# Performance work log

Measured on AMD Instinct MI355X. Metric: run time of the kernel, lower is better.

The kernel has to match this reference:

```python
import jax, jax.numpy as jnp
import numpy as np
import math

B, L, D = 2, 2048, 1024
H, KV, HD = 16, 4, 64          # num_heads, num_kv_heads, head_dim
GROUPS = H // KV
ROPE_BASE = 10000.0


def _alibi_slopes(n_heads):
    def pow2(n):
        start = 2.0 ** (-(2.0 ** (-(math.log2(n) - 3))))
        return [start * (start ** i) for i in range(n)]
    if math.log2(n_heads).is_integer():
        return pow2(n_heads)
    c = 2 ** math.floor(math.log2(n_heads))
    return pow2(c) + _alibi_slopes(2 * c)[0::2][: n_heads - c]


def _rope_cos_sin(seq_len, dim, dtype):
    inv_freq = 1.0 / (ROPE_BASE ** (jnp.arange(0, dim, 2, dtype=jnp.float32) / dim))
    t = jnp.arange(seq_len, dtype=jnp.float32)
    freqs = t[:, None] * inv_freq[None, :]          # [L, dim/2]
    emb = jnp.concatenate([freqs, freqs], axis=-1)  # [L, dim]
    return jnp.cos(emb).astype(dtype), jnp.sin(emb).astype(dtype)


def _rotate_half(x):
    x1, x2 = x[..., : x.shape[-1] // 2], x[..., x.shape[-1] // 2 :]
    return jnp.concatenate([-x2, x1], axis=-1)


def setup_inputs() -> dict:
    key = jax.random.key(0)
    ks = jax.random.split(key, 5)
    s = 0.02
    return {
        "x": jax.random.normal(ks[0], (B, L, D), jnp.float32),
        "Wq": jax.random.normal(ks[1], (D, H * HD), jnp.float32) * s,
        "Wk": jax.random.normal(ks[2], (D, KV * HD), jnp.float32) * s,
        "Wv": jax.random.normal(ks[3], (D, KV * HD), jnp.float32) * s,
        "Wo": jax.random.normal(ks[4], (H * HD, D), jnp.float32) * s,
    }


def reference(x, Wq, Wk, Wv, Wo):
    b, l, _ = x.shape
    q = (x @ Wq).reshape(b, l, H, HD).transpose(0, 2, 1, 3)   # [B,H,L,hd]
    k = (x @ Wk).reshape(b, l, KV, HD).transpose(0, 2, 1, 3)  # [B,KV,L,hd]
    v = (x @ Wv).reshape(b, l, KV, HD).transpose(0, 2, 1, 3)
    # MQA broadcast: repeat_interleave over head dim
    k = jnp.repeat(k, GROUPS, axis=1)  # [B,H,L,hd]
    v = jnp.repeat(v, GROUPS, axis=1)

    cos, sin = _rope_cos_sin(l, HD, x.dtype)  # [L,hd]
    q = q * cos + _rotate_half(q) * sin
    k = k * cos + _rotate_half(k) * sin

    attn = jnp.einsum("bhqd,bhkd->bhqk", q, k) / math.sqrt(HD)
    # ALiBi bias: (j - i) * slope_h
    pos = jnp.arange(l)
    rel = (pos[None, :] - pos[:, None]).astype(x.dtype)        # [L,L]
    slopes = jnp.asarray(_alibi_slopes(H), dtype=x.dtype)      # [H]
    attn = attn + slopes[None, :, None, None] * rel[None, None, :, :]

    attn = jax.nn.softmax(attn, axis=-1)
    out = jnp.einsum("bhqk,bhkd->bhqd", attn, v)               # [B,H,L,hd]
    out = out.transpose(0, 2, 1, 3).reshape(b, l, H * HD)
    return out @ Wo
```

## Files before the change

kernel.cpp:

```cpp
#include <hip/hip_runtime.h>
#include <math.h>

typedef unsigned short u16;
typedef unsigned int u32;
typedef __attribute__((ext_vector_type(8))) short short8;
typedef __attribute__((ext_vector_type(4))) short short4v;
typedef __attribute__((ext_vector_type(4))) float floatx4;
typedef __attribute__((ext_vector_type(2))) unsigned int uint2v;

#define HN 16
#define KVN 4
#define HDN 64
#define BN_ 2
#define LN 2048
#define DN 1024

__device__ __forceinline__ u16 f2bf(float f) {
    u32 u = __float_as_uint(f);
    u32 r = (u + 0x7fffu + ((u >> 16) & 1u)) >> 16;
    return (u16)r;
}

__device__ __forceinline__ u32 pack2bf(float f0, float f1) {
    u32 u0 = __float_as_uint(f0);
    u32 u1 = __float_as_uint(f1);
    u0 += 0x7fffu + ((u0 >> 16) & 1u);
    u1 += 0x7fffu + ((u1 >> 16) & 1u);
    return __builtin_amdgcn_perm(u1, u0, 0x07060302u);
}

__device__ __forceinline__ void gl16(const u16* g, u16* l) {
    __builtin_amdgcn_global_load_lds(
        (const __attribute__((address_space(1))) u32*)g,
        (__attribute__((address_space(3))) u32*)l, 16, 0, 0);
}

__device__ __forceinline__ void do_transpose(const float* __restrict__ W, u16* __restrict__ WT,
                                             int R, int C, int bx, int by, int tid,
                                             float (*t)[33]) {
    int tx = tid & 31, ty = tid >> 5;
    int c0 = bx * 32, r0 = by * 32;
#pragma unroll
    for (int i = 0; i < 4; i++) {
        int r = r0 + ty + i * 8;
        t[ty + i * 8][tx] = W[(size_t)r * C + c0 + tx];
    }
    __syncthreads();
#pragma unroll
    for (int i = 0; i < 4; i++) {
        int c = c0 + ty + i * 8;
        WT[(size_t)c * R + r0 + tx] = f2bf(t[tx][ty + i * 8]);
    }
}

__global__ __launch_bounds__(256) void prep_kernel(const float* __restrict__ x,
                                                   const float* __restrict__ Wq,
                                                   const float* __restrict__ Wk,
                                                   const float* __restrict__ Wv,
                                                   const float* __restrict__ Wo,
                                                   u16* __restrict__ xb,
                                                   u16* __restrict__ WT,
                                                   u16* __restrict__ WoT) {
    __shared__ float t[32][33];
    int blk = blockIdx.x, tid = threadIdx.x;
    if (blk < 4096) {
        int i = blk * 256 + tid;
        floatx4 v = ((const floatx4*)x)[i];
        short4v o;
        o[0] = (short)f2bf(v[0]);
        o[1] = (short)f2bf(v[1]);
        o[2] = (short)f2bf(v[2]);
        o[3] = (short)f2bf(v[3]);
        ((short4v*)xb)[i] = o;
    } else if (blk < 5120) {
        int z = blk - 4096;
        do_transpose(Wq, WT, 1024, 1024, z & 31, z >> 5, tid, t);
    } else if (blk < 5376) {
        int z = blk - 5120;
        do_transpose(Wk, WT + 1024 * 1024, 1024, 256, z & 7, z >> 3, tid, t);
    } else if (blk < 5632) {
        int z = blk - 5376;
        do_transpose(Wv, WT + 1280 * 1024, 1024, 256, z & 7, z >> 3, tid, t);
    } else {
        int z = blk - 5632;
        do_transpose(Wo, WoT, 1024, 1024, z & 31, z >> 5, tid, t);
    }
}

__global__ __launch_bounds__(256) void gemm_qkv_rope(const u16* __restrict__ A,
                                                     const u16* __restrict__ BT,
                                                     u16* __restrict__ Qb,
                                                     u16* __restrict__ Kb,
                                                     u16* __restrict__ Vt) {
    __shared__ u16 sm[16384];
    const int K = 1024;
    int tid = threadIdx.x;
    int w = tid >> 6, l = tid & 63, quad = l >> 4, l16 = l & 15;
    int wm = (w >> 1) * 64, wn = (w & 1) * 64;
    floatx4 acc[4][4];
#pragma unroll
    for (int i = 0; i < 4; i++)
#pragma unroll
        for (int j = 0; j < 4; j++) acc[i][j] = (floatx4){0.f, 0.f, 0.f, 0.f};
    const u16* ag0 = A + (size_t)(blockIdx.y * 128 + (tid >> 2)) * K + (tid & 3) * 8;
    const u16* ag1 = ag0 + (size_t)64 * K;
    const u16* bg0 = BT + (size_t)(blockIdx.x * 128 + (tid >> 2)) * K + (tid & 3) * 8;
    const u16* bg1 = bg0 + (size_t)64 * K;
    int lbase = tid * 8;
    gl16(ag0, &sm[lbase]);
    gl16(ag1, &sm[2048 + lbase]);
    gl16(bg0, &sm[4096 + lbase]);
    gl16(bg1, &sm[6144 + lbase]);
    for (int it = 0; it < 32; it++) {
        __syncthreads();
        int cur = it & 1;
        if (it + 1 < 32) {
            int nb = (cur ^ 1) * 8192;
            ag0 += 32; ag1 += 32; bg0 += 32; bg1 += 32;
            gl16(ag0, &sm[nb + lbase]);
            gl16(ag1, &sm[nb + 2048 + lbase]);
            gl16(bg0, &sm[nb + 4096 + lbase]);
            gl16(bg1, &sm[nb + 6144 + lbase]);
        }
        const u16* sa = &sm[cur * 8192];
        const u16* sb = sa + 4096;
        short8 af[4], bfr[4];
#pragma unroll
        for (int mt = 0; mt < 4; mt++) af[mt] = *(const short8*)&sa[(wm + mt * 16 + l16) * 32 + quad * 8];
#pragma unroll
        for (int nt = 0; nt < 4; nt++) bfr[nt] = *(const short8*)&sb[(wn + nt * 16 + l16) * 32 + quad * 8];
#pragma unroll
        for (int mt = 0; mt < 4; mt++)
#pragma unroll
            for (int nt = 0; nt < 4; nt++)
                acc[mt][nt] = __builtin_amdgcn_mfma_f32_16x16x32_bf16(af[mt], bfr[nt], acc[mt][nt], 0, 0, 0);
    }
    int bx = blockIdx.x;
    int row0 = blockIdx.y * 128 + wm;
    const float L2R32 = 0.4152410118609203f;
    if (bx < 10) {
        int isK = (bx >= 8);
        int head = isK ? ((bx - 8) * 2 + (w & 1)) : (bx * 2 + (w & 1));
        u16* dst = isK ? (Kb + ((size_t)head) * LN * HDN) : (Qb + ((size_t)head) * LN * HDN);
        size_t bstride = (size_t)(isK ? KVN : HN) * LN * HDN;
        float invf[2];
#pragma unroll
        for (int ntp = 0; ntp < 2; ntp++) invf[ntp] = exp2f(-(float)(ntp * 16 + l16) * L2R32);
#pragma unroll
        for (int mt = 0; mt < 4; mt++)
#pragma unroll
            for (int r = 0; r < 4; r++) {
                int row = row0 + mt * 16 + quad * 4 + r;
                int b = row >> 11;
                int lpos = row & 2047;
                float lf = (float)lpos;
#pragma unroll
                for (int ntp = 0; ntp < 2; ntp++) {
                    float th = lf * invf[ntp];
                    float s, c;
                    __sincosf(th, &s, &c);
                    float x1 = acc[mt][ntp][r], x2 = acc[mt][ntp + 2][r];
                    size_t base = (size_t)b * bstride + ((size_t)lpos) * HDN + ntp * 16 + l16;
                    dst[base] = f2bf(x1 * c - x2 * s);
                    dst[base + 32] = f2bf(x2 * c + x1 * s);
                }
            }
    } else {
        int kv = (bx - 10) * 2 + (w & 1);
#pragma unroll
        for (int mt = 0; mt < 4; mt++)
#pragma unroll
            for (int r = 0; r < 4; r++) {
                int row = row0 + mt * 16 + quad * 4 + r;
                int b = row >> 11;
                int lpos = row & 2047;
#pragma unroll
                for (int nt = 0; nt < 4; nt++) {
                    int d = nt * 16 + l16;
                    Vt[(((size_t)b * KVN + kv) * HDN + d) * LN + lpos] = f2bf(acc[mt][nt][r]);
                }
            }
    }
}

__global__ __launch_bounds__(256) void gemm_bf16_f32(const u16* __restrict__ A,
                                                     const u16* __restrict__ BT,
                                                     float* __restrict__ C,
                                                     int M, int N, int K) {
    __shared__ u16 sm[12288];
    int tid = threadIdx.x;
    int w = tid >> 6, l = tid & 63, quad = l >> 4, l16 = l & 15;
    int wm = (w >> 1) * 64, wn = (w & 1) * 32;
    floatx4 acc[4][2];
#pragma unroll
    for (int i = 0; i < 4; i++)
#pragma unroll
        for (int j = 0; j < 2; j++) acc[i][j] = (floatx4){0.f, 0.f, 0.f, 0.f};
    const u16* ag0 = A + (size_t)(blockIdx.y * 128 + 16 * w + (l >> 2)) * K + (l & 3) * 8;
    const u16* ag1 = ag0 + (size_t)64 * K;
    const u16* bg = BT + (size_t)(blockIdx.x * 64 + 16 * w + (l >> 2)) * K + (l & 3) * 8;
    int lbase = w * 512 + l * 8;
    gl16(ag0, &sm[lbase]);
    gl16(ag1, &sm[2048 + lbase]);
    gl16(bg, &sm[4096 + lbase]);
    int nit = K >> 5;
    for (int it = 0; it < nit; it++) {
        __syncthreads();
        int cur = it & 1;
        if (it + 1 < nit) {
            int nb = (cur ^ 1) * 6144;
            ag0 += 32; ag1 += 32; bg += 32;
            gl16(ag0, &sm[nb + lbase]);
            gl16(ag1, &sm[nb + 2048 + lbase]);
            gl16(bg, &sm[nb + 4096 + lbase]);
        }
        const u16* smc = &sm[cur * 6144];
        short8 af[4], bfr[2];
#pragma unroll
        for (int mt = 0; mt < 4; mt++) af[mt] = *(const short8*)&smc[(wm + mt * 16 + l16) * 32 + quad * 8];
#pragma unroll
        for (int nt = 0; nt < 2; nt++) bfr[nt] = *(const short8*)&smc[4096 + (wn + nt * 16 + l16) * 32 + quad * 8];
#pragma unroll
        for (int mt = 0; mt < 4; mt++)
#pragma unroll
            for (int nt = 0; nt < 2; nt++)
                acc[mt][nt] = __builtin_amdgcn_mfma_f32_16x16x32_bf16(af[mt], bfr[nt], acc[mt][nt], 0, 0, 0);
    }
#pragma unroll
    for (int mt = 0; mt < 4; mt++)
#pragma unroll
        for (int nt = 0; nt < 2; nt++)
#pragma unroll
            for (int r = 0; r < 4; r++) {
                int row = blockIdx.y * 128 + wm + mt * 16 + quad * 4 + r;
                int col = blockIdx.x * 64 + wn + nt * 16 + l16;
                C[(size_t)row * N + col] = acc[mt][nt][r];
            }
}

static __device__ const signed char hs_tab[16] = {15, 14, 13, 12, 11, 10, 9, 8,
                                                  0, 1, 2, 3, 4, 5, 6, 7};
static __device__ const signed char nit_tab[16] = {32, 32, 32, 32, 32, 24, 17, 12,
                                                   1, 2, 2, 3, 3, 5, 6, 9};

__global__ __launch_bounds__(256) void attention_kernel(const u16* __restrict__ Qb,
                                                        const u16* __restrict__ Kb,
                                                        const u16* __restrict__ Vt,
                                                        u16* __restrict__ AO) {
    __shared__ u16 sm[20992];
    int rank = blockIdx.x >> 5, sub = blockIdx.x & 31;
    int h = hs_tab[rank], nit = nit_tab[rank];
    int ks0 = LN - nit * 64;
    int b = sub >> 4, qb = sub & 15;
    int kv = h >> 2;
    int tid = threadIdx.x, w = tid >> 6, l = tid & 63, quad = l >> 4, l16 = l & 15;
    const u16* Kbase = Kb + (((size_t)b * KVN + kv) * LN) * HDN;
    const u16* Vbase = Vt + (((size_t)b * KVN + kv) * HDN) * LN;
    short8 bq[2][2];
#pragma unroll
    for (int t = 0; t < 2; t++) {
        const u16* Qrow = Qb + (((size_t)b * HN + h) * LN + qb * 128 + t * 64 + w * 16 + l16) * HDN;
        bq[t][0] = *(const short8*)&Qrow[quad * 8];
        bq[t][1] = *(const short8*)&Qrow[32 + quad * 8];
    }
    const float LOG2E = 1.4426950408889634f;
    float sLE = exp2f(-0.5f * (float)(h + 1)) * LOG2E;
    float c1 = 0.125f * LOG2E;
    float koff[4][4];
#pragma unroll
    for (int nt = 0; nt < 4; nt++)
#pragma unroll
        for (int r = 0; r < 4; r++)
            koff[nt][r] = fmaf(sLE, (float)(ks0 + nt * 16 + quad * 4 + r - (LN - 1)), -17.312340491f);
    float kbrun = 0.0f, kstep = 64.0f * sLE;
    floatx4 O[2][4], lacc[2];
#pragma unroll
    for (int t = 0; t < 2; t++) {
        lacc[t] = (floatx4){0.f, 0.f, 0.f, 0.f};
#pragma unroll
        for (int md = 0; md < 4; md++) O[t][md] = (floatx4){0.f, 0.f, 0.f, 0.f};
    }
    short8 ones;
#pragma unroll
    for (int z = 0; z < 8; z++) ones[z] = (short)0x3F80;
    u16* pb = &sm[16384 + w * 1152];
    int lbase = w * 512 + l * 8;
    const u16* kg = Kbase + (size_t)(ks0 + 16 * w + (l >> 2)) * 64 + (l & 3) * 8;
    const u16* vg = Vbase + (size_t)(16 * w + (l >> 2)) * 2048 + ks0 + (l & 3) * 8;
    gl16(kg, &sm[lbase]);
    gl16(kg + 32, &sm[2048 + lbase]);
    gl16(vg, &sm[8192 + lbase]);
    gl16(vg + 32, &sm[8192 + 2048 + lbase]);
    for (int it = 0; it < nit; it++) {
        __syncthreads();
        int cur = it & 1;
        if (it + 1 < nit) {
            int nb = (cur ^ 1) * 4096;
            kg += 4096;
            vg += 64;
            gl16(kg, &sm[nb + lbase]);
            gl16(kg + 32, &sm[nb + 2048 + lbase]);
            gl16(vg, &sm[8192 + nb + lbase]);
            gl16(vg + 32, &sm[8192 + nb + 2048 + lbase]);
        }
        const u16* kc = &sm[cur * 4096];
        const u16* vc = &sm[8192 + cur * 4096];
        short8 ak0[4], ak1[4], av0[4], av1[4];
#pragma unroll
        for (int nt = 0; nt < 4; nt++) {
            ak0[nt] = *(const short8*)&kc[(nt * 16 + l16) * 32 + quad * 8];
            ak1[nt] = *(const short8*)&kc[2048 + (nt * 16 + l16) * 32 + quad * 8];
        }
#pragma unroll
        for (int md = 0; md < 4; md++) {
            av0[md] = *(const short8*)&vc[(md * 16 + l16) * 32 + quad * 8];
            av1[md] = *(const short8*)&vc[2048 + (md * 16 + l16) * 32 + quad * 8];
        }
        float koff2[4][4];
#pragma unroll
        for (int nt = 0; nt < 4; nt++)
#pragma unroll
            for (int r = 0; r < 4; r++) koff2[nt][r] = koff[nt][r] + kbrun;
        kbrun += kstep;
#pragma unroll
        for (int t = 0; t < 2; t++) {
            floatx4 S[4];
#pragma unroll
            for (int nt = 0; nt < 4; nt++) {
                floatx4 sa = (floatx4){0.f, 0.f, 0.f, 0.f};
                sa = __builtin_amdgcn_mfma_f32_16x16x32_bf16(ak0[nt], bq[t][0], sa, 0, 0, 0);
                sa = __builtin_amdgcn_mfma_f32_16x16x32_bf16(ak1[nt], bq[t][1], sa, 0, 0, 0);
                S[nt] = sa;
            }
#pragma unroll
            for (int nt = 0; nt < 4; nt++) {
                float p0 = __builtin_amdgcn_exp2f(S[nt][0] * c1 + koff2[nt][0]);
                float p1 = __builtin_amdgcn_exp2f(S[nt][1] * c1 + koff2[nt][1]);
                float p2 = __builtin_amdgcn_exp2f(S[nt][2] * c1 + koff2[nt][2]);
                float p3 = __builtin_amdgcn_exp2f(S[nt][3] * c1 + koff2[nt][3]);
                uint2v pk;
                pk[0] = pack2bf(p0, p1);
                pk[1] = pack2bf(p2, p3);
                *(uint2v*)&pb[l16 * 72 + nt * 16 + quad * 4] = pk;
            }
            short8 bp0 = *(const short8*)&pb[l16 * 72 + quad * 8];
            short8 bp1 = *(const short8*)&pb[l16 * 72 + 32 + quad * 8];
#pragma unroll
            for (int md = 0; md < 4; md++) {
                O[t][md] = __builtin_amdgcn_mfma_f32_16x16x32_bf16(av0[md], bp0, O[t][md], 0, 0, 0);
                O[t][md] = __builtin_amdgcn_mfma_f32_16x16x32_bf16(av1[md], bp1, O[t][md], 0, 0, 0);
            }
            lacc[t] = __builtin_amdgcn_mfma_f32_16x16x32_bf16(ones, bp0, lacc[t], 0, 0, 0);
            lacc[t] = __builtin_amdgcn_mfma_f32_16x16x32_bf16(ones, bp1, lacc[t], 0, 0, 0);
        }
    }
#pragma unroll
    for (int t = 0; t < 2; t++) {
        float inv = 1.0f / lacc[t][0];
        int qg = qb * 128 + t * 64 + w * 16 + l16;
        size_t base = ((size_t)b * LN + qg) * 1024 + h * 64 + quad * 4;
#pragma unroll
        for (int md = 0; md < 4; md++) {
            uint2v pk;
            pk[0] = pack2bf(O[t][md][0] * inv, O[t][md][1] * inv);
            pk[1] = pack2bf(O[t][md][2] * inv, O[t][md][3] * inv);
            *(uint2v*)&AO[base + md * 16] = pk;
        }
    }
}

extern "C" void kernel_launch(void* const* d_in, const int* in_sizes, int n_in,
                              void* d_out, int out_size, void* d_ws, size_t ws_size,
                              hipStream_t stream) {
    const float* x = (const float*)d_in[0];
    const float* Wq = (const float*)d_in[1];
    const float* Wk = (const float*)d_in[2];
    const float* Wv = (const float*)d_in[3];
    const float* Wo = (const float*)d_in[4];
    float* out = (float*)d_out;
    char* ws = (char*)d_ws;
    u16* xb = (u16*)(ws);
    u16* WT = (u16*)(ws + 8388608);
    u16* WoT = (u16*)(ws + 11534336);
    u16* Qb = (u16*)(ws + 13631488);
    u16* Kb = (u16*)(ws + 22020096);
    u16* Vt = (u16*)(ws + 24117248);
    u16* AO = xb;

    prep_kernel<<<6656, 256, 0, stream>>>(x, Wq, Wk, Wv, Wo, xb, WT, WoT);
    gemm_qkv_rope<<<dim3(12, 32), 256, 0, stream>>>(xb, WT, Qb, Kb, Vt);
    attention_kernel<<<512, 256, 0, stream>>>(Qb, Kb, Vt, AO);
    gemm_bf16_f32<<<dim3(1024 / 64, 4096 / 128), 256, 0, stream>>>(AO, WoT, out, 4096, 1024, 1024);
}
```

Baseline: 163.1 us.

## Halve tile sizes in QKV GEMM and attention to double block counts

The QKV+RoPE GEMM moves from 128x128 to 128x64 tiles, so each block owns one head and the grid has 768 blocks instead of 384. The attention kernel now handles 64 query rows per block instead of 128, launching 1024 blocks. The output GEMM switches from a 2x2 to a 4x1 wave layout. The aim is better CU occupancy and load balance on a large GPU, at the cost of reloading K/V and weight tiles more often per output.

```diff
diff --git a/kernel.cpp b/kernel.cpp
--- a/kernel.cpp
+++ b/kernel.cpp
@@ -92,45 +92,42 @@
                                                      u16* __restrict__ Qb,
                                                      u16* __restrict__ Kb,
                                                      u16* __restrict__ Vt) {
-    __shared__ u16 sm[16384];
+    __shared__ u16 sm[12288];
     const int K = 1024;
     int tid = threadIdx.x;
     int w = tid >> 6, l = tid & 63, quad = l >> 4, l16 = l & 15;
-    int wm = (w >> 1) * 64, wn = (w & 1) * 64;
-    floatx4 acc[4][4];
-#pragma unroll
-    for (int i = 0; i < 4; i++)
+    int wm = w * 32;
+    floatx4 acc[2][4];
+#pragma unroll
+    for (int i = 0; i < 2; i++)
 #pragma unroll
         for (int j = 0; j < 4; j++) acc[i][j] = (floatx4){0.f, 0.f, 0.f, 0.f};
     const u16* ag0 = A + (size_t)(blockIdx.y * 128 + (tid >> 2)) * K + (tid & 3) * 8;
     const u16* ag1 = ag0 + (size_t)64 * K;
-    const u16* bg0 = BT + (size_t)(blockIdx.x * 128 + (tid >> 2)) * K + (tid & 3) * 8;
-    const u16* bg1 = bg0 + (size_t)64 * K;
+    const u16* bg = BT + (size_t)(blockIdx.x * 64 + (tid >> 2)) * K + (tid & 3) * 8;
     int lbase = tid * 8;
     gl16(ag0, &sm[lbase]);
     gl16(ag1, &sm[2048 + lbase]);
-    gl16(bg0, &sm[4096 + lbase]);
-    gl16(bg1, &sm[6144 + lbase]);
+    gl16(bg, &sm[4096 + lbase]);
     for (int it = 0; it < 32; it++) {
         __syncthreads();
         int cur = it & 1;
         if (it + 1 < 32) {
-            int nb = (cur ^ 1) * 8192;
-            ag0 += 32; ag1 += 32; bg0 += 32; bg1 += 32;
+            int nb = (cur ^ 1) * 6144;
+            ag0 += 32; ag1 += 32; bg += 32;
             gl16(ag0, &sm[nb + lbase]);
             gl16(ag1, &sm[nb + 2048 + lbase]);
-            gl16(bg0, &sm[nb + 4096 + lbase]);
-            gl16(bg1, &sm[nb + 6144 + lbase]);
-        }
-        const u16* sa = &sm[cur * 8192];
+            gl16(bg, &sm[nb + 4096 + lbase]);
+        }
+        const u16* sa = &sm[cur * 6144];
         const u16* sb = sa + 4096;
-        short8 af[4], bfr[4];
-#pragma unroll
-        for (int mt = 0; mt < 4; mt++) af[mt] = *(const short8*)&sa[(wm + mt * 16 + l16) * 32 + quad * 8];
-#pragma unroll
-        for (int nt = 0; nt < 4; nt++) bfr[nt] = *(const short8*)&sb[(wn + nt * 16 + l16) * 32 + quad * 8];
-#pragma unroll
-        for (int mt = 0; mt < 4; mt++)
+        short8 af[2], bfr[4];
+#pragma unroll
+        for (int mt = 0; mt < 2; mt++) af[mt] = *(const short8*)&sa[(wm + mt * 16 + l16) * 32 + quad * 8];
+#pragma unroll
+        for (int nt = 0; nt < 4; nt++) bfr[nt] = *(const short8*)&sb[(nt * 16 + l16) * 32 + quad * 8];
+#pragma unroll
+        for (int mt = 0; mt < 2; mt++)
 #pragma unroll
             for (int nt = 0; nt < 4; nt++)
                 acc[mt][nt] = __builtin_amdgcn_mfma_f32_16x16x32_bf16(af[mt], bfr[nt], acc[mt][nt], 0, 0, 0);
@@ -138,16 +135,17 @@
     int bx = blockIdx.x;
     int row0 = blockIdx.y * 128 + wm;
     const float L2R32 = 0.4152410118609203f;
-    if (bx < 10) {
-        int isK = (bx >= 8);
-        int head = isK ? ((bx - 8) * 2 + (w & 1)) : (bx * 2 + (w & 1));
-        u16* dst = isK ? (Kb + ((size_t)head) * LN * HDN) : (Qb + ((size_t)head) * LN * HDN);
+    if (bx < 20) {
+        int isK = (bx >= 16);
+        int head = isK ? (bx - 16) : bx;
+        u16* dst = isK ? Kb : Qb;
         size_t bstride = (size_t)(isK ? KVN : HN) * LN * HDN;
         float invf[2];
 #pragma unroll
         for (int ntp = 0; ntp < 2; ntp++) invf[ntp] = exp2f(-(float)(ntp * 16 + l16) * L2R32);
-#pragma unroll
-        for (int mt = 0; mt < 4; mt++)
+        dst += (size_t)head * LN * HDN;
+#pragma unroll
+        for (int mt = 0; mt < 2; mt++)
 #pragma unroll
             for (int r = 0; r < 4; r++) {
                 int row = row0 + mt * 16 + quad * 4 + r;
@@ -166,9 +164,9 @@
                 }
             }
     } else {
-        int kv = (bx - 10) * 2 + (w & 1);
-#pragma unroll
-        for (int mt = 0; mt < 4; mt++)
+        int kv = bx - 20;
+#pragma unroll
+        for (int mt = 0; mt < 2; mt++)
 #pragma unroll
             for (int r = 0; r < 4; r++) {
                 int row = row0 + mt * 16 + quad * 4 + r;
@@ -183,59 +181,60 @@
     }
 }
 
-__global__ __launch_bounds__(256) void gemm_bf16_f32(const u16* __restrict__ A,
-                                                     const u16* __restrict__ BT,
-                                                     float* __restrict__ C,
-                                                     int M, int N, int K) {
+__global__ __launch_bounds__(256) void gemm_out(const u16* __restrict__ A,
+                                                const u16* __restrict__ BT,
+                                                float* __restrict__ C) {
     __shared__ u16 sm[12288];
+    const int K = 1024, N = 1024;
     int tid = threadIdx.x;
     int w = tid >> 6, l = tid & 63, quad = l >> 4, l16 = l & 15;
-    int wm = (w >> 1) * 64, wn = (w & 1) * 32;
-    floatx4 acc[4][2];
-#pragma unroll
-    for (int i = 0; i < 4; i++)
-#pragma unroll
-        for (int j = 0; j < 2; j++) acc[i][j] = (floatx4){0.f, 0.f, 0.f, 0.f};
-    const u16* ag0 = A + (size_t)(blockIdx.y * 128 + 16 * w + (l >> 2)) * K + (l & 3) * 8;
+    int wm = w * 32;
+    floatx4 acc[2][4];
+#pragma unroll
+    for (int i = 0; i < 2; i++)
+#pragma unroll
+        for (int j = 0; j < 4; j++) acc[i][j] = (floatx4){0.f, 0.f, 0.f, 0.f};
+    const u16* ag0 = A + (size_t)(blockIdx.y * 128 + (tid >> 2)) * K + (tid & 3) * 8;
     const u16* ag1 = ag0 + (size_t)64 * K;
-    const u16* bg = BT + (size_t)(blockIdx.x * 64 + 16 * w + (l >> 2)) * K + (l & 3) * 8;
-    int lbase = w * 512 + l * 8;
+    const u16* bg = BT + (size_t)(blockIdx.x * 64 + (tid >> 2)) * K + (tid & 3) * 8;
+    int lbase = tid * 8;
     gl16(ag0, &sm[lbase]);
     gl16(ag1, &sm[2048 + lbase]);
     gl16(bg, &sm[4096 + lbase]);
-    int nit = K >> 5;
-    for (int it = 0; it < nit; it++) {
+    for (int it = 0; it < 32; it++) {
         __syncthreads();
         int cur = it & 1;
-        if (it + 1 < nit) {
+        if (it + 1 < 32) {
             int nb = (cur ^ 1) * 6144;
             ag0 += 32; ag1 += 32; bg += 32;
             gl16(ag0, &sm[nb + lbase]);
             gl16(ag1, &sm[nb + 2048 + lbase]);
             gl16(bg, &sm[nb + 4096 + lbase]);
         }
-        const u16* smc = &sm[cur * 6144];
-        short8 af[4], bfr[2];
-#pragma unroll
-        for (int mt = 0; mt < 4; mt++) af[mt] = *(const short8*)&smc[(wm + mt * 16 + l16) * 32 + quad * 8];
-#pragma unroll
-        for (int nt = 0; nt < 2; nt++) bfr[nt] = *(const short8*)&smc[4096 + (wn + nt * 16 + l16) * 32 + quad * 8];
-#pragma unroll
-        for (int mt = 0; mt < 4; mt++)
-#pragma unroll
-            for (int nt = 0; nt < 2; nt++)
+        const u16* sa = &sm[cur * 6144];
+        const u16* sb = sa + 4096;
+        short8 af[2], bfr[4];
+#pragma unroll
+        for (int mt = 0; mt < 2; mt++) af[mt] = *(const short8*)&sa[(wm + mt * 16 + l16) * 32 + quad * 8];
+#pragma unroll
+        for (int nt = 0; nt < 4; nt++) bfr[nt] = *(const short8*)&sb[(nt * 16 + l16) * 32 + quad * 8];
+#pragma unroll
+        for (int mt = 0; mt < 2; mt++)
+#pragma unroll
+            for (int nt = 0; nt < 4; nt++)
                 acc[mt][nt] = __builtin_amdgcn_mfma_f32_16x16x32_bf16(af[mt], bfr[nt], acc[mt][nt], 0, 0, 0);
     }
 #pragma unroll
-    for (int mt = 0; mt < 4; mt++)
-#pragma unroll
-        for (int nt = 0; nt < 2; nt++)
-#pragma unroll
-            for (int r = 0; r < 4; r++) {
-                int row = blockIdx.y * 128 + wm + mt * 16 + quad * 4 + r;
-                int col = blockIdx.x * 64 + wn + nt * 16 + l16;
+    for (int mt = 0; mt < 2; mt++)
+#pragma unroll
+        for (int r = 0; r < 4; r++) {
+            int row = blockIdx.y * 128 + wm + mt * 16 + quad * 4 + r;
+#pragma unroll
+            for (int nt = 0; nt < 4; nt++) {
+                int col = blockIdx.x * 64 + nt * 16 + l16;
                 C[(size_t)row * N + col] = acc[mt][nt][r];
             }
+        }
 }
 
 static __device__ const signed char hs_tab[16] = {15, 14, 13, 12, 11, 10, 9, 8,
@@ -248,21 +247,17 @@
                                                         const u16* __restrict__ Vt,
                                                         u16* __restrict__ AO) {
     __shared__ u16 sm[20992];
-    int rank = blockIdx.x >> 5, sub = blockIdx.x & 31;
+    int rank = blockIdx.x >> 6, sub = blockIdx.x & 63;
     int h = hs_tab[rank], nit = nit_tab[rank];
     int ks0 = LN - nit * 64;
-    int b = sub >> 4, qb = sub & 15;
+    int b = sub >> 5, qb = sub & 31;
     int kv = h >> 2;
     int tid = threadIdx.x, w = tid >> 6, l = tid & 63, quad = l >> 4, l16 = l & 15;
     const u16* Kbase = Kb + (((size_t)b * KVN + kv) * LN) * HDN;
     const u16* Vbase = Vt + (((size_t)b * KVN + kv) * HDN) * LN;
-    short8 bq[2][2];
-#pragma unroll
-    for (int t = 0; t < 2; t++) {
-        const u16* Qrow = Qb + (((size_t)b * HN + h) * LN + qb * 128 + t * 64 + w * 16 + l16) * HDN;
-        bq[t][0] = *(const short8*)&Qrow[quad * 8];
-        bq[t][1] = *(const short8*)&Qrow[32 + quad * 8];
-    }
+    const u16* Qrow = Qb + (((size_t)b * HN + h) * LN + qb * 64 + w * 16 + l16) * HDN;
+    short8 bq0 = *(const short8*)&Qrow[quad * 8];
+    short8 bq1 = *(const short8*)&Qrow[32 + quad * 8];
     const float LOG2E = 1.4426950408889634f;
     float sLE = exp2f(-0.5f * (float)(h + 1)) * LOG2E;
     float c1 = 0.125f * LOG2E;
@@ -273,13 +268,10 @@
         for (int r = 0; r < 4; r++)
             koff[nt][r] = fmaf(sLE, (float)(ks0 + nt * 16 + quad * 4 + r - (LN - 1)), -17.312340491f);
     float kbrun = 0.0f, kstep = 64.0f * sLE;
-    floatx4 O[2][4], lacc[2];
-#pragma unroll
-    for (int t = 0; t < 2; t++) {
-        lacc[t] = (floatx4){0.f, 0.f, 0.f, 0.f};
-#pragma unroll
-        for (int md = 0; md < 4; md++) O[t][md] = (floatx4){0.f, 0.f, 0.f, 0.f};
-    }
+    floatx4 O[4], lacc;
+    lacc = (floatx4){0.f, 0.f, 0.f, 0.f};
+#pragma unroll
+    for (int md = 0; md < 4; md++) O[md] = (floatx4){0.f, 0.f, 0.f, 0.f};
     short8 ones;
 #pragma unroll
     for (int z = 0; z < 8; z++) ones[z] = (short)0x3F80;
@@ -316,56 +308,45 @@
             av0[md] = *(const short8*)&vc[(md * 16 + l16) * 32 + quad * 8];
             av1[md] = *(const short8*)&vc[2048 + (md * 16 + l16) * 32 + quad * 8];
         }
-        float koff2[4][4];
-#pragma unroll
-        for (int nt = 0; nt < 4; nt++)
-#pragma unroll
-            for (int r = 0; r < 4; r++) koff2[nt][r] = koff[nt][r] + kbrun;
+        floatx4 S[4];
+#pragma unroll
+        for (int nt = 0; nt < 4; nt++) {
+            floatx4 sa = (floatx4){0.f, 0.f, 0.f, 0.f};
+            sa = __builtin_amdgcn_mfma_f32_16x16x32_bf16(ak0[nt], bq0, sa, 0, 0, 0);
+            sa = __builtin_amdgcn_mfma_f32_16x16x32_bf16(ak1[nt], bq1, sa, 0, 0, 0);
+            S[nt] = sa;
+        }
+#pragma unroll
+        for (int nt = 0; nt < 4; nt++) {
+            float p0 = __builtin_amdgcn_exp2f(S[nt][0] * c1 + (koff[nt][0] + kbrun));
+            float p1 = __builtin_amdgcn_exp2f(S[nt][1] * c1 + (koff[nt][1] + kbrun));
+            float p2 = __builtin_amdgcn_exp2f(S[nt][2] * c1 + (koff[nt][2] + kbrun));
+            float p3 = __builtin_amdgcn_exp2f(S[nt][3] * c1 + (koff[nt][3] + kbrun));
+            uint2v pk;
+            pk[0] = pack2bf(p0, p1);
+            pk[1] = pack2bf(p2, p3);
+            *(uint2v*)&pb[l16 * 72 + nt * 16 + quad * 4] = pk;
+        }
         kbrun += kstep;
-#pragma unroll
-        for (int t = 0; t < 2; t++) {
-            floatx4 S[4];
-#pragma unroll
-            for (int nt = 0; nt < 4; nt++) {
-                floatx4 sa = (floatx4){0.f, 0.f, 0.f, 0.f};
-                sa = __builtin_amdgcn_mfma_f32_16x16x32_bf16(ak0[nt], bq[t][0], sa, 0, 0, 0);
-                sa = __builtin_amdgcn_mfma_f32_16x16x32_bf16(ak1[nt], bq[t][1], sa, 0, 0, 0);
-                S[nt] = sa;
-            }
-#pragma unroll
-            for (int nt = 0; nt < 4; nt++) {
-                float p0 = __builtin_amdgcn_exp2f(S[nt][0] * c1 + koff2[nt][0]);
-                float p1 = __builtin_amdgcn_exp2f(S[nt][1] * c1 + koff2[nt][1]);
-                float p2 = __builtin_amdgcn_exp2f(S[nt][2] * c1 + koff2[nt][2]);
-                float p3 = __builtin_amdgcn_exp2f(S[nt][3] * c1 + koff2[nt][3]);
-                uint2v pk;
-                pk[0] = pack2bf(p0, p1);
-                pk[1] = pack2bf(p2, p3);
-                *(uint2v*)&pb[l16 * 72 + nt * 16 + quad * 4] = pk;
-            }
-            short8 bp0 = *(const short8*)&pb[l16 * 72 + quad * 8];
-            short8 bp1 = *(const short8*)&pb[l16 * 72 + 32 + quad * 8];
-#pragma unroll
-            for (int md = 0; md < 4; md++) {
-                O[t][md] = __builtin_amdgcn_mfma_f32_16x16x32_bf16(av0[md], bp0, O[t][md], 0, 0, 0);
-                O[t][md] = __builtin_amdgcn_mfma_f32_16x16x32_bf16(av1[md], bp1, O[t][md], 0, 0, 0);
-            }
-            lacc[t] = __builtin_amdgcn_mfma_f32_16x16x32_bf16(ones, bp0, lacc[t], 0, 0, 0);
-            lacc[t] = __builtin_amdgcn_mfma_f32_16x16x32_bf16(ones, bp1, lacc[t], 0, 0, 0);
-        }
-    }
-#pragma unroll
-    for (int t = 0; t < 2; t++) {
-        float inv = 1.0f / lacc[t][0];
-        int qg = qb * 128 + t * 64 + w * 16 + l16;
-        size_t base = ((size_t)b * LN + qg) * 1024 + h * 64 + quad * 4;
+        short8 bp0 = *(const short8*)&pb[l16 * 72 + quad * 8];
+        short8 bp1 = *(const short8*)&pb[l16 * 72 + 32 + quad * 8];
 #pragma unroll
         for (int md = 0; md < 4; md++) {
-            uint2v pk;
-            pk[0] = pack2bf(O[t][md][0] * inv, O[t][md][1] * inv);
-            pk[1] = pack2bf(O[t][md][2] * inv, O[t][md][3] * inv);
-            *(uint2v*)&AO[base + md * 16] = pk;
-        }
+            O[md] = __builtin_amdgcn_mfma_f32_16x16x32_bf16(av0[md], bp0, O[md], 0, 0, 0);
+            O[md] = __builtin_amdgcn_mfma_f32_16x16x32_bf16(av1[md], bp1, O[md], 0, 0, 0);
+        }
+        lacc = __builtin_amdgcn_mfma_f32_16x16x32_bf16(ones, bp0, lacc, 0, 0, 0);
+        lacc = __builtin_amdgcn_mfma_f32_16x16x32_bf16(ones, bp1, lacc, 0, 0, 0);
+    }
+    float inv = 1.0f / lacc[0];
+    int qg = qb * 64 + w * 16 + l16;
+    size_t base = ((size_t)b * LN + qg) * 1024 + h * 64 + quad * 4;
+#pragma unroll
+    for (int md = 0; md < 4; md++) {
+        uint2v pk;
+        pk[0] = pack2bf(O[md][0] * inv, O[md][1] * inv);
+        pk[1] = pack2bf(O[md][2] * inv, O[md][3] * inv);
+        *(uint2v*)&AO[base + md * 16] = pk;
     }
 }
 
@@ -388,7 +369,7 @@
     u16* AO = xb;
 
     prep_kernel<<<6656, 256, 0, stream>>>(x, Wq, Wk, Wv, Wo, xb, WT, WoT);
-    gemm_qkv_rope<<<dim3(12, 32), 256, 0, stream>>>(xb, WT, Qb, Kb, Vt);
-    attention_kernel<<<512, 256, 0, stream>>>(Qb, Kb, Vt, AO);
-    gemm_bf16_f32<<<dim3(1024 / 64, 4096 / 128), 256, 0, stream>>>(AO, WoT, out, 4096, 1024, 1024);
-}
+    gemm_qkv_rope<<<dim3(24, 32), 256, 0, stream>>>(xb, WT, Qb, Kb, Vt);
+    attention_kernel<<<1024, 256, 0, stream>>>(Qb, Kb, Vt, AO);
+    gemm_out<<<dim3(16, 32), 256, 0, stream>>>(AO, WoT, out);
+}
```

Result: no change. 161.3 us (-1.1%).
